# Performance work log

Measured on AMD Instinct MI355X. Metric: run time of the kernel, lower is better.

Reference implementation:

```python
import jax, jax.numpy as jnp
import numpy as np

DIM = 2048
NUM_HEADS = 32
NUM_KV_HEADS = 8
HEAD_DIM = DIM // NUM_HEADS           # 64
KV_REPEAT = NUM_HEADS // NUM_KV_HEADS  # 4
KV_DIM = HEAD_DIM * NUM_KV_HEADS      # 512
THRESHOLD = 0.05


def _init_weight(key, out_f, in_f):
    # kaiming_uniform(a=sqrt(5)) ~ U(-1/sqrt(in_f), 1/sqrt(in_f))
    bound = 1.0 / np.sqrt(in_f)
    return jax.random.uniform(key, (out_f, in_f), jnp.float32, -bound, bound)


def ternarize_ste(w):
    scale = jnp.maximum(jnp.abs(w).mean(), 1e-6)
    t = jnp.where(w > THRESHOLD * scale, 1.0,
                  jnp.where(w < -THRESHOLD * scale, -1.0, 0.0))
    return w + jax.lax.stop_gradient(t - w)


def setup_inputs() -> dict:
    key = jax.random.key(0)
    kx, kq, kk, kv, ko = jax.random.split(key, 5)
    x = jax.random.normal(kx, (2, 2048, DIM), jnp.float32)
    wq = _init_weight(kq, DIM, DIM)
    wk = _init_weight(kk, KV_DIM, DIM)
    wv = _init_weight(kv, KV_DIM, DIM)
    wo = _init_weight(ko, DIM, DIM)
    return {"x": x, "wq": wq, "wk": wk, "wv": wv, "wo": wo}


def reference(x, wq, wk, wv, wo):
    b, s, _ = x.shape
    g, r, d = NUM_KV_HEADS, KV_REPEAT, HEAD_DIM
    q = x @ ternarize_ste(wq).T   # [b,s,dim]
    k = x @ ternarize_ste(wk).T   # [b,s,kv_dim]
    v = x @ ternarize_ste(wv).T   # [b,s,kv_dim]
    # group heads as (kv_group g, repeat r) to avoid physically expanding KV
    q = q.reshape(b, s, g, r, d)
    k = k.reshape(b, s, g, d)
    v = v.reshape(b, s, g, d)
    att = jnp.einsum('bqgrd,bkgd->bgrqk', q, k) / np.sqrt(d).astype(jnp.float32)
    causal = jnp.tril(jnp.ones((s, s), dtype=bool))  # [q,k] keep lower tri
    att = jnp.where(causal, att, -jnp.inf)
    probs = jax.nn.softmax(att, axis=-1)
    out = jnp.einsum('bgrqk,bkgd->bqgrd', probs, v).reshape(b, s, DIM)
    return out @ ternarize_ste(wo).T
```

## Files before the change

kernel.cpp:

```cpp
#include <hip/hip_runtime.h>
#include <hip/hip_bf16.h>
#include <stdint.h>

#define DIMN 2048
#define KVD  512
#define NH   32
#define BATCH 2
#define SEQ  2048
#define ROWS (BATCH*SEQ)
#define NT   (SEQ/64)

typedef __attribute__((ext_vector_type(4))) float f32x4;
typedef __attribute__((ext_vector_type(8))) short bf16x8;

__device__ __forceinline__ float bf2f(short s){
  union{uint32_t u;float f;} v; v.u=((uint32_t)(uint16_t)s)<<16; return v.f;
}
__device__ __forceinline__ short f2bf_rn(float f){
  __hip_bfloat16 h = __float2bfloat16(f);
  short s; __builtin_memcpy(&s, &h, 2); return s;
}
__device__ __forceinline__ f32x4 mfma16(bf16x8 a, bf16x8 b, f32x4 c){
  return __builtin_amdgcn_mfma_f32_16x16x32_bf16(a,b,c,0,0,0);
}
__device__ __forceinline__ short ternbf(float v, float thr){
  return v > thr ? (short)0x3F80 : (v < -thr ? (short)0xBF80 : (short)0);
}
__device__ __forceinline__ void gload16(const short* g, short* l){
  __builtin_amdgcn_global_load_lds(
      (const __attribute__((address_space(1))) uint32_t*)g,
      (__attribute__((address_space(3))) uint32_t*)l, 16, 0, 0);
}

__global__ void k_abssum4(const float* __restrict__ w0, const float* __restrict__ w1,
                          const float* __restrict__ w2, const float* __restrict__ w3,
                          float* __restrict__ partial){
  __shared__ float red[256];
  const float* ptrs[4] = {w0, w1, w2, w3};
  const int ns[4] = {DIMN*DIMN, KVD*DIMN, KVD*DIMN, DIMN*DIMN};
  const int wi = blockIdx.y;
  const float* w = ptrs[wi];
  const int n = ns[wi];
  float s = 0.f;
  for (int i = blockIdx.x*256 + threadIdx.x; i < n; i += 256*gridDim.x) s += fabsf(w[i]);
  red[threadIdx.x] = s; __syncthreads();
  for (int o = 128; o > 0; o >>= 1){
    if (threadIdx.x < o) red[threadIdx.x] += red[threadIdx.x+o];
    __syncthreads();
  }
  if (threadIdx.x == 0) partial[wi*256 + blockIdx.x] = red[0];
}

__global__ void k_scales(const float* __restrict__ partial, float* __restrict__ scales){
  __shared__ float red[256];
  int t = threadIdx.x;
  const int counts[4] = {DIMN*DIMN, KVD*DIMN, KVD*DIMN, DIMN*DIMN};
  for (int wi = 0; wi < 4; wi++){
    red[t] = partial[wi*256 + t]; __syncthreads();
    for (int o = 128; o > 0; o >>= 1){
      if (t < o) red[t] += red[t+o];
      __syncthreads();
    }
    if (t == 0){
      float mean = red[0] / (float)counts[wi];
      scales[wi] = 0.05f * fmaxf(mean, 1e-6f);
    }
    __syncthreads();
  }
}

__global__ void k_prep_x(const float* __restrict__ x, short* __restrict__ hi,
                         short* __restrict__ lo){
  long i = ((long)blockIdx.x*256 + threadIdx.x)*8;
  f32x4 a = *(const f32x4*)(x+i);
  f32x4 b = *(const f32x4*)(x+i+4);
  bf16x8 h, l;
  #pragma unroll
  for (int j = 0; j < 4; j++){
    short p = f2bf_rn(a[j]); h[j]   = p; l[j]   = f2bf_rn(a[j]-bf2f(p));
    short q = f2bf_rn(b[j]); h[4+j] = q; l[4+j] = f2bf_rn(b[j]-bf2f(q));
  }
  *(bf16x8*)(hi+i) = h;
  *(bf16x8*)(lo+i) = l;
}

__global__ void k_tern4(const float* __restrict__ w0, const float* __restrict__ w1,
                        const float* __restrict__ w2, const float* __restrict__ w3,
                        short* __restrict__ o0, short* __restrict__ o1,
                        short* __restrict__ o2, short* __restrict__ o3,
                        const float* __restrict__ scales){
  const float* ws[4] = {w0, w1, w2, w3};
  short* os[4] = {o0, o1, o2, o3};
  const int ns[4] = {DIMN*DIMN, KVD*DIMN, KVD*DIMN, DIMN*DIMN};
  const int wi = blockIdx.y;
  long i = ((long)blockIdx.x*256 + threadIdx.x)*8;
  if (i >= ns[wi]) return;
  const float thr = scales[wi];
  const float* w = ws[wi];
  f32x4 a = *(const f32x4*)(w+i);
  f32x4 b = *(const f32x4*)(w+i+4);
  bf16x8 t;
  #pragma unroll
  for (int j = 0; j < 4; j++){
    t[j]   = ternbf(a[j], thr);
    t[4+j] = ternbf(b[j], thr);
  }
  *(bf16x8*)(os[wi]+i) = t;
}

template<int SPLITA, int SPLITB, int OUTF32>
__device__ __forceinline__ void gemm_core(
    const short* __restrict__ Ahg, const short* __restrict__ Xlg,
    const short* __restrict__ Bg,
    float* __restrict__ Of, short* __restrict__ Oh, short* __restrict__ Ol,
    bool writelo, int N, int K, int bn, int bm,
    short (*AhS)[64], short (*XlS)[64], short (*BsS)[64]){
  const int tid = threadIdx.x, lane = tid & 63, w = tid >> 6;
  const int wr = w >> 1, wc = w & 1;
  const int la = lane & 15, kg = lane >> 4;
  const int xrb = SPLITA ? bm : bn;
  f32x4 acc[4][4] = {};
  for (int k0 = 0; k0 < K; k0 += 64){
    #pragma unroll
    for (int j = 0; j < 4; j++){
      const int flat = (w*4 + j)*64 + lane;
      const int row = flat >> 3, c16 = (flat & 7)*8;
      short* lb = &AhS[0][0] + (w*4 + j)*512;
      gload16(Ahg + (long)(bm+row)*K + k0 + c16, lb);
    }
    if constexpr (SPLITA || SPLITB){
      #pragma unroll
      for (int j = 0; j < 4; j++){
        const int flat = (w*4 + j)*64 + lane;
        const int row = flat >> 3, c16 = (flat & 7)*8;
        short* lb = &XlS[0][0] + (w*4 + j)*512;
        gload16(Xlg + (long)(xrb+row)*K + k0 + c16, lb);
      }
    }
    #pragma unroll
    for (int j = 0; j < 4; j++){
      const int flat = (w*4 + j)*64 + lane;
      const int row = flat >> 3, c16 = (flat & 7)*8;
      short* lb = &BsS[0][0] + (w*4 + j)*512;
      gload16(Bg + (long)(bn+row)*K + k0 + c16, lb);
    }
    __syncthreads();
    #pragma unroll
    for (int ks = 0; ks < 2; ks++){
      bf16x8 af[4], bfr[4];
      #pragma unroll
      for (int mi = 0; mi < 4; mi++)
        af[mi] = *(bf16x8*)&AhS[wr*64 + mi*16 + la][ks*32 + kg*8];
      #pragma unroll
      for (int ni = 0; ni < 4; ni++)
        bfr[ni] = *(bf16x8*)&BsS[wc*64 + ni*16 + la][ks*32 + kg*8];
      #pragma unroll
      for (int mi = 0; mi < 4; mi++)
        #pragma unroll
        for (int ni = 0; ni < 4; ni++)
          acc[mi][ni] = mfma16(af[mi], bfr[ni], acc[mi][ni]);
      if constexpr (SPLITA){
        bf16x8 alf[4];
        #pragma unroll
        for (int mi = 0; mi < 4; mi++)
          alf[mi] = *(bf16x8*)&XlS[wr*64 + mi*16 + la][ks*32 + kg*8];
        #pragma unroll
        for (int mi = 0; mi < 4; mi++)
          #pragma unroll
          for (int ni = 0; ni < 4; ni++)
            acc[mi][ni] = mfma16(alf[mi], bfr[ni], acc[mi][ni]);
      }
      if constexpr (SPLITB){
        bf16x8 blf[4];
        #pragma unroll
        for (int ni = 0; ni < 4; ni++)
          blf[ni] = *(bf16x8*)&XlS[wc*64 + ni*16 + la][ks*32 + kg*8];
        #pragma unroll
        for (int mi = 0; mi < 4; mi++)
          #pragma unroll
          for (int ni = 0; ni < 4; ni++)
            acc[mi][ni] = mfma16(af[mi], blf[ni], acc[mi][ni]);
      }
    }
    __syncthreads();
  }
  #pragma unroll
  for (int mi = 0; mi < 4; mi++)
    #pragma unroll
    for (int ni = 0; ni < 4; ni++)
      #pragma unroll
      for (int rr = 0; rr < 4; rr++){
        long row = bm + wr*64 + mi*16 + kg*4 + rr;
        long col = bn + wc*64 + ni*16 + la;
        float v = acc[mi][ni][rr];
        if constexpr (OUTF32){
          Of[row*(long)N + col] = v;
        } else {
          short hb = f2bf_rn(v);
          Oh[row*(long)N + col] = hb;
          if (writelo)
            Ol[row*(long)N + col] = f2bf_rn(v - bf2f(hb));
        }
      }
}

__global__ __launch_bounds__(256) void k_gemm_q(
    const short* __restrict__ Ahg, const short* __restrict__ Alg,
    const short* __restrict__ Bg, short* __restrict__ Oh, short* __restrict__ Ol,
    int N, int K){
  __shared__ short S0[128][64];
  __shared__ short S1[128][64];
  __shared__ short S2[128][64];
  gemm_core<1,0,0>(Ahg, Alg, Bg, nullptr, Oh, Ol, true, N, K,
                   blockIdx.x*128, blockIdx.y*128, S0, S1, S2);
}

__global__ __launch_bounds__(256) void k_gemm_kvt(
    const short* __restrict__ xhi, const short* __restrict__ xlo,
    const short* __restrict__ wkT, const short* __restrict__ wvT,
    short* __restrict__ KOh, short* __restrict__ KOl, short* __restrict__ VT,
    int K){
  __shared__ short S0[128][64];
  __shared__ short S1[128][64];
  __shared__ short S2[128][64];
  if (blockIdx.z == 0){
    gemm_core<1,0,0>(xhi, xlo, wkT, nullptr, KOh, KOl, true, KVD, K,
                     blockIdx.x*128, blockIdx.y*128, S0, S1, S2);
  } else {
    gemm_core<0,1,0>(wvT, xlo, xhi, nullptr, VT, nullptr, false, ROWS, K,
                     blockIdx.y*128, blockIdx.x*128, S0, S1, S2);
  }
}

__global__ __launch_bounds__(256) void k_gemm_o(
    const short* __restrict__ Ahg, const short* __restrict__ Bg,
    float* __restrict__ Of, int N, int K){
  __shared__ short S0[128][64];
  __shared__ short S2[128][64];
  gemm_core<0,0,1>(Ahg, nullptr, Bg, Of, nullptr, nullptr, false, N, K,
                   blockIdx.x*128, blockIdx.y*128, S0, nullptr, S2);
}

__global__ __launch_bounds__(256) void k_attn(
    const short* __restrict__ qhi, const short* __restrict__ qlo,
    const short* __restrict__ khi, const short* __restrict__ klo,
    const short* __restrict__ vT, short* __restrict__ attout){
  __shared__ short Kh[64][68];
  __shared__ short Kl[64][68];
  __shared__ short Vt[64][68];
  __shared__ short P[64][68];
  const int qp = blockIdx.x, h = blockIdx.y, b = blockIdx.z;
  const int g = h >> 2;
  const int tid = threadIdx.x, w = tid >> 6, lane = tid & 63;
  const int la = lane & 15, kg = lane >> 4;
  const int trow = tid >> 2, tcol = (tid & 3) * 16;

  for (int phase = 0; phase < 2; phase++){
    const int qt = phase ? (NT - 1 - qp) : qp;
    const int qbase = qt*64;

    bf16x8 qh[2], ql[2];
    {
      long qrow = (long)(b*SEQ + qbase + w*16 + la);
      #pragma unroll
      for (int ks = 0; ks < 2; ks++){
        long off = qrow*DIMN + h*64 + ks*32 + kg*8;
        qh[ks] = *(const bf16x8*)(qhi + off);
        ql[ks] = *(const bf16x8*)(qlo + off);
      }
    }
    f32x4 Oacc[4] = {};
    float m[4], l[4];
    #pragma unroll
    for (int r = 0; r < 4; r++){ m[r] = -INFINITY; l[r] = 0.f; }

    for (int kt = 0; kt <= qt; kt++){
      __syncthreads();
      {
        const short* ksrc  = khi + (long)(b*SEQ + kt*64 + trow)*KVD + g*64 + tcol;
        const short* klsrc = klo + (long)(b*SEQ + kt*64 + trow)*KVD + g*64 + tcol;
        const short* vsrc  = vT  + (long)(g*64 + trow)*ROWS + b*SEQ + kt*64 + tcol;
        *(bf16x8*)&Kh[trow][tcol]   = *(const bf16x8*)ksrc;
        *(bf16x8*)&Kh[trow][tcol+8] = *(const bf16x8*)(ksrc + 8);
        *(bf16x8*)&Kl[trow][tcol]   = *(const bf16x8*)klsrc;
        *(bf16x8*)&Kl[trow][tcol+8] = *(const bf16x8*)(klsrc + 8);
        *(bf16x8*)&Vt[trow][tcol]   = *(const bf16x8*)vsrc;
        *(bf16x8*)&Vt[trow][tcol+8] = *(const bf16x8*)(vsrc + 8);
      }
      __syncthreads();

      f32x4 s[4];
      __builtin_amdgcn_s_setprio(1);
      #pragma unroll
      for (int ni = 0; ni < 4; ni++){
        f32x4 a = {0.f,0.f,0.f,0.f};
        #pragma unroll
        for (int ks = 0; ks < 2; ks++){
          bf16x8 kh = *(bf16x8*)&Kh[ni*16 + la][ks*32 + kg*8];
          bf16x8 kl = *(bf16x8*)&Kl[ni*16 + la][ks*32 + kg*8];
          a = mfma16(qh[ks], kh, a);
          a = mfma16(ql[ks], kh, a);
          a = mfma16(qh[ks], kl, a);
        }
        s[ni] = a;
      }
      __builtin_amdgcn_s_setprio(0);

      const bool lastTile = (kt == qt);
      #pragma unroll
      for (int ni = 0; ni < 4; ni++)
        #pragma unroll
        for (int r = 0; r < 4; r++){
          float v = s[ni][r] * 0.125f;
          if (lastTile){
            int kc = kt*64 + ni*16 + la;
            int qr = qbase + w*16 + kg*4 + r;
            if (kc > qr) v = -INFINITY;
          }
          s[ni][r] = v;
        }

      float ef[4];
      #pragma unroll
      for (int r = 0; r < 4; r++){
        float v = fmaxf(fmaxf(s[0][r], s[1][r]), fmaxf(s[2][r], s[3][r]));
        for (int o = 1; o < 16; o <<= 1) v = fmaxf(v, __shfl_xor(v, o, 64));
        float mn = fmaxf(m[r], v);
        ef[r] = __expf(m[r] - mn);
        m[r] = mn;
      }
      #pragma unroll
      for (int r = 0; r < 4; r++){
        float rs = 0.f;
        #pragma unroll
        for (int ni = 0; ni < 4; ni++){
          float p = __expf(s[ni][r] - m[r]);
          s[ni][r] = p;
          rs += p;
        }
        for (int o = 1; o < 16; o <<= 1) rs += __shfl_xor(rs, o, 64);
        l[r] = l[r]*ef[r] + rs;
      }
      #pragma unroll
      for (int d = 0; d < 4; d++)
        #pragma unroll
        for (int r = 0; r < 4; r++) Oacc[d][r] *= ef[r];

      #pragma unroll
      for (int ni = 0; ni < 4; ni++)
        #pragma unroll
        for (int r = 0; r < 4; r++)
          P[w*16 + kg*4 + r][ni*16 + la] = f2bf_rn(s[ni][r]);

      __builtin_amdgcn_s_setprio(1);
      #pragma unroll
      for (int ks = 0; ks < 2; ks++){
        bf16x8 pa = *(bf16x8*)&P[w*16 + la][ks*32 + kg*8];
        #pragma unroll
        for (int d = 0; d < 4; d++){
          bf16x8 vb = *(bf16x8*)&Vt[d*16 + la][ks*32 + kg*8];
          Oacc[d] = mfma16(pa, vb, Oacc[d]);
        }
      }
      __builtin_amdgcn_s_setprio(0);
    }

    #pragma unroll
    for (int d = 0; d < 4; d++)
      #pragma unroll
      for (int r = 0; r < 4; r++){
        float v = Oacc[d][r] / l[r];
        long row = (long)(b*SEQ + qbase + w*16 + kg*4 + r);
        attout[row*DIMN + h*64 + d*16 + la] = f2bf_rn(v);
      }
    __syncthreads();
  }
}

extern "C" void kernel_launch(void* const* d_in, const int* in_sizes, int n_in,
                              void* d_out, int out_size, void* d_ws, size_t ws_size,
                              hipStream_t stream){
  const float* x  = (const float*)d_in[0];
  const float* wq = (const float*)d_in[1];
  const float* wk = (const float*)d_in[2];
  const float* wv = (const float*)d_in[3];
  const float* wo = (const float*)d_in[4];
  float* out = (float*)d_out;
  char* ws = (char*)d_ws;

  const size_t SZ_QD = (size_t)ROWS*DIMN*2;
  const size_t SZ_KD = (size_t)ROWS*KVD*2;
  const size_t SZ_WQ = (size_t)DIMN*DIMN*2;
  const size_t SZ_WK = (size_t)KVD*DIMN*2;
  const size_t NEED = 65536 + 2*SZ_QD + 2*SZ_WQ + 2*SZ_WK + 2*SZ_QD + 3*SZ_KD;
  if (ws_size < NEED) return;

  float* scales   = (float*)ws;
  float* partials = (float*)(ws + 1024);
  size_t off = 65536;
  auto alloc = [&](size_t bytes)->char*{
    char* p = ws + off; off += (bytes + 255) & ~(size_t)255; return p;
  };
  short* xhi = (short*)alloc(SZ_QD);
  short* xlo = (short*)alloc(SZ_QD);
  short* wqT = (short*)alloc(SZ_WQ);
  short* wkT = (short*)alloc(SZ_WK);
  short* wvT = (short*)alloc(SZ_WK);
  short* woT = (short*)alloc(SZ_WQ);
  short* qhib = (short*)alloc(SZ_QD);
  short* qlob = (short*)alloc(SZ_QD);
  short* khib = (short*)alloc(SZ_KD);
  short* klob = (short*)alloc(SZ_KD);
  short* vTb  = (short*)alloc(SZ_KD);
  short* atto = xhi;

  {
    dim3 g(256, 4);
    k_abssum4<<<g,256,0,stream>>>(wq, wk, wv, wo, partials);
  }
  k_scales<<<1,256,0,stream>>>(partials, scales);

  {
    dim3 g(2048, 4);
    k_tern4<<<g,256,0,stream>>>(wq, wk, wv, wo, wqT, wkT, wvT, woT, scales);
  }
  k_prep_x<<<4096,256,0,stream>>>(x, xhi, xlo);

  {
    dim3 g(DIMN/128, ROWS/128);
    k_gemm_q<<<g,256,0,stream>>>(xhi, xlo, wqT, qhib, qlob, DIMN, DIMN);
  }
  {
    dim3 g(KVD/128, ROWS/128, 2);
    k_gemm_kvt<<<g,256,0,stream>>>(xhi, xlo, wkT, wvT, khib, klob, vTb, DIMN);
  }

  {
    dim3 g(NT/2, NH, BATCH);
    k_attn<<<g,256,0,stream>>>(qhib, qlob, khib, klob, vTb, atto);
  }

  {
    dim3 g(DIMN/128, ROWS/128);
    k_gemm_o<<<g,256,0,stream>>>(atto, woT, out, DIMN, DIMN);
  }
}
```

Before: 499.9 us.

## Prefetch next KV tile into registers, drop V lo-pass, use manual bf16 rounding

The attention loop now loads the next K/V tile into registers while computing on the current tile in LDS, so global latency overlaps with MFMA and softmax work. LDS row padding changes from 68 to 72 shorts, which alters the bank-conflict pattern. The V projection drops the x-lo correction term, halving its MFMAs at some cost in precision. A bit-trick bf16 round-to-nearest-even replaces the library conversion in several places to cut conversion overhead, though it does not handle NaN.

```diff
diff --git a/kernel.cpp b/kernel.cpp
--- a/kernel.cpp
+++ b/kernel.cpp
@@ -15,6 +15,10 @@
 
 __device__ __forceinline__ float bf2f(short s){
   union{uint32_t u;float f;} v; v.u=((uint32_t)(uint16_t)s)<<16; return v.f;
+}
+__device__ __forceinline__ short f2bf(float f){
+  union{float f;uint32_t u;} v; v.f=f;
+  uint32_t r=(v.u + 0x7fffu + ((v.u>>16)&1u))>>16; return (short)r;
 }
 __device__ __forceinline__ short f2bf_rn(float f){
   __hip_bfloat16 h = __float2bfloat16(f);
@@ -77,8 +81,8 @@
   bf16x8 h, l;
   #pragma unroll
   for (int j = 0; j < 4; j++){
-    short p = f2bf_rn(a[j]); h[j]   = p; l[j]   = f2bf_rn(a[j]-bf2f(p));
-    short q = f2bf_rn(b[j]); h[4+j] = q; l[4+j] = f2bf_rn(b[j]-bf2f(q));
+    short p = f2bf(a[j]); h[j]   = p; l[j]   = f2bf(a[j]-bf2f(p));
+    short q = f2bf(b[j]); h[4+j] = q; l[4+j] = f2bf(b[j]-bf2f(q));
   }
   *(bf16x8*)(hi+i) = h;
   *(bf16x8*)(lo+i) = l;
@@ -227,7 +231,7 @@
     gemm_core<1,0,0>(xhi, xlo, wkT, nullptr, KOh, KOl, true, KVD, K,
                      blockIdx.x*128, blockIdx.y*128, S0, S1, S2);
   } else {
-    gemm_core<0,1,0>(wvT, xlo, xhi, nullptr, VT, nullptr, false, ROWS, K,
+    gemm_core<0,0,0>(wvT, nullptr, xhi, nullptr, VT, nullptr, false, ROWS, K,
                      blockIdx.y*128, blockIdx.x*128, S0, S1, S2);
   }
 }
@@ -245,10 +249,10 @@
     const short* __restrict__ qhi, const short* __restrict__ qlo,
     const short* __restrict__ khi, const short* __restrict__ klo,
     const short* __restrict__ vT, short* __restrict__ attout){
-  __shared__ short Kh[64][68];
-  __shared__ short Kl[64][68];
-  __shared__ short Vt[64][68];
-  __shared__ short P[64][68];
+  __shared__ short Kh[64][72];
+  __shared__ short Kl[64][72];
+  __shared__ short Vt[64][72];
+  __shared__ short P[64][72];
   const int qp = blockIdx.x, h = blockIdx.y, b = blockIdx.z;
   const int g = h >> 2;
   const int tid = threadIdx.x, w = tid >> 6, lane = tid & 63;
@@ -274,20 +278,35 @@
     #pragma unroll
     for (int r = 0; r < 4; r++){ m[r] = -INFINITY; l[r] = 0.f; }
 
+    bf16x8 rkh0, rkh1, rkl0, rkl1, rvt0, rvt1;
+    {
+      const short* ksrc  = khi + (long)(b*SEQ + trow)*KVD + g*64 + tcol;
+      const short* klsrc = klo + (long)(b*SEQ + trow)*KVD + g*64 + tcol;
+      const short* vsrc  = vT  + (long)(g*64 + trow)*ROWS + b*SEQ + tcol;
+      rkh0 = *(const bf16x8*)ksrc;    rkh1 = *(const bf16x8*)(ksrc + 8);
+      rkl0 = *(const bf16x8*)klsrc;   rkl1 = *(const bf16x8*)(klsrc + 8);
+      rvt0 = *(const bf16x8*)vsrc;    rvt1 = *(const bf16x8*)(vsrc + 8);
+    }
+
     for (int kt = 0; kt <= qt; kt++){
       __syncthreads();
+      *(bf16x8*)&Kh[trow][tcol]   = rkh0;
+      *(bf16x8*)&Kh[trow][tcol+8] = rkh1;
+      *(bf16x8*)&Kl[trow][tcol]   = rkl0;
+      *(bf16x8*)&Kl[trow][tcol+8] = rkl1;
+      *(bf16x8*)&Vt[trow][tcol]   = rvt0;
+      *(bf16x8*)&Vt[trow][tcol+8] = rvt1;
+      __syncthreads();
+
       {
-        const short* ksrc  = khi + (long)(b*SEQ + kt*64 + trow)*KVD + g*64 + tcol;
-        const short* klsrc = klo + (long)(b*SEQ + kt*64 + trow)*KVD + g*64 + tcol;
-        const short* vsrc  = vT  + (long)(g*64 + trow)*ROWS + b*SEQ + kt*64 + tcol;
-        *(bf16x8*)&Kh[trow][tcol]   = *(const bf16x8*)ksrc;
-        *(bf16x8*)&Kh[trow][tcol+8] = *(const bf16x8*)(ksrc + 8);
-        *(bf16x8*)&Kl[trow][tcol]   = *(const bf16x8*)klsrc;
-        *(bf16x8*)&Kl[trow][tcol+8] = *(const bf16x8*)(klsrc + 8);
-        *(bf16x8*)&Vt[trow][tcol]   = *(const bf16x8*)vsrc;
-        *(bf16x8*)&Vt[trow][tcol+8] = *(const bf16x8*)(vsrc + 8);
-      }
-      __syncthreads();
+        const int ktn = (kt < qt) ? (kt + 1) : qt;
+        const short* ksrc  = khi + (long)(b*SEQ + ktn*64 + trow)*KVD + g*64 + tcol;
+        const short* klsrc = klo + (long)(b*SEQ + ktn*64 + trow)*KVD + g*64 + tcol;
+        const short* vsrc  = vT  + (long)(g*64 + trow)*ROWS + b*SEQ + ktn*64 + tcol;
+        rkh0 = *(const bf16x8*)ksrc;    rkh1 = *(const bf16x8*)(ksrc + 8);
+        rkl0 = *(const bf16x8*)klsrc;   rkl1 = *(const bf16x8*)(klsrc + 8);
+        rvt0 = *(const bf16x8*)vsrc;    rvt1 = *(const bf16x8*)(vsrc + 8);
+      }
 
       f32x4 s[4];
       __builtin_amdgcn_s_setprio(1);
@@ -350,7 +369,7 @@
       for (int ni = 0; ni < 4; ni++)
         #pragma unroll
         for (int r = 0; r < 4; r++)
-          P[w*16 + kg*4 + r][ni*16 + la] = f2bf_rn(s[ni][r]);
+          P[w*16 + kg*4 + r][ni*16 + la] = f2bf(s[ni][r]);
 
       __builtin_amdgcn_s_setprio(1);
       #pragma unroll
@@ -371,7 +390,7 @@
       for (int r = 0; r < 4; r++){
         float v = Oacc[d][r] / l[r];
         long row = (long)(b*SEQ + qbase + w*16 + kg*4 + r);
-        attout[row*DIMN + h*64 + d*16 + la] = f2bf_rn(v);
+        attout[row*DIMN + h*64 + d*16 + la] = f2bf(v);
       }
     __syncthreads();
   }
```

Result: no change. 491.3 us (-1.7%).
